# Optimization experiments

Measured on AMD Instinct MI355X. Metric: run time of the kernel, lower is better.

The kernel has to match this reference:

```python
import jax, jax.numpy as jnp
import numpy as np

B, T, S, I, H = 128, 256, 256, 512, 512


def setup_inputs() -> dict:
    key = jax.random.key(0)
    ks = jax.random.split(key, 10)
    sc = 0.02
    return {
        "x": jax.random.normal(ks[0], (B, T, I), jnp.float32),
        "h0": jax.random.normal(ks[1], (B, H), jnp.float32),
        "c0": jax.random.normal(ks[2], (B, H), jnp.float32),
        "ctx": jax.random.normal(ks[3], (S, B, H), jnp.float32),
        "Wi": jax.random.normal(ks[4], (4 * H, I), jnp.float32) * sc,
        "bi": jax.random.normal(ks[5], (4 * H,), jnp.float32) * sc,
        "Wh": jax.random.normal(ks[6], (4 * H, H), jnp.float32) * sc,
        "bh": jax.random.normal(ks[7], (4 * H,), jnp.float32) * sc,
        "W_in": jax.random.normal(ks[8], (H, H), jnp.float32) * sc,
        "W_out": jax.random.normal(ks[9], (H, 2 * H), jnp.float32) * sc,
    }


def reference(x, h0, c0, ctx, Wi, bi, Wh, bh, W_in, W_out):
    ctx_b = jnp.transpose(ctx, (1, 0, 2))  # [B, S, H]

    def step(carry, xt):
        hx, cx = carry
        gates = xt @ Wi.T + bi + hx @ Wh.T + bh  # [B, 4H]
        i_g, f_g, g_g, o_g = jnp.split(gates, 4, axis=1)
        cy = jax.nn.sigmoid(f_g) * cx + jax.nn.sigmoid(i_g) * jnp.tanh(g_g)
        hy = jax.nn.sigmoid(o_g) * jnp.tanh(cy)
        # soft dot attention
        target = hy @ W_in.T                              # [B, H]
        attn = jax.nn.softmax(jnp.einsum('bsh,bh->bs', ctx_b, target), axis=1)
        wc = jnp.einsum('bs,bsh->bh', attn, ctx_b)        # [B, H]
        h_tilde = jnp.tanh(jnp.concatenate([wc, hy], axis=1) @ W_out.T)
        return (h_tilde, cy), h_tilde

    (hf, cf), outs = jax.lax.scan(step, (h0, c0), jnp.transpose(x, (1, 0, 2)))
    output = jnp.transpose(outs, (1, 0, 2))  # [B, T, H] (batch_first)
    return output, hf, cf
```

## Files before the change

kernel.cpp:

```cpp
#include <hip/hip_runtime.h>
#include <hip/hip_bf16.h>
#include <stdint.h>

#define B_ 128
#define T_ 256
#define S_ 256
#define I_ 512
#define H_ 512
#define RSLOT 32

typedef __attribute__((ext_vector_type(8))) short short8;
typedef __attribute__((ext_vector_type(4))) float f32x4;
typedef unsigned short ushort_t;

__device__ __forceinline__ float bf2f(ushort_t u){
  union{ unsigned int i; float f;} v; v.i = ((unsigned int)u)<<16; return v.f;
}
__device__ __forceinline__ ushort_t f2bf(float f){
  union{ unsigned int i; float f;} v; v.f=f;
  unsigned int x=v.i; unsigned int r = x + 0x7fffu + ((x>>16)&1u);
  return (ushort_t)(r>>16);
}
__device__ __forceinline__ float sigm(float x){ return 1.f/(1.f + __expf(-x)); }
__device__ __forceinline__ float tanh_s(float x){
  float a = fabsf(x);
  float e = __expf(-2.f*a);
  float t = (1.f - e)/(1.f + e);
  return x < 0.f ? -t : t;
}

__device__ __forceinline__ f32x4 MFMA16(short8 a, short8 b, f32x4 c){
  typedef __attribute__((ext_vector_type(8))) __bf16 bf16x8;
  return __builtin_amdgcn_mfma_f32_16x16x32_bf16(
      __builtin_bit_cast(bf16x8, a), __builtin_bit_cast(bf16x8, b), c, 0, 0, 0);
}

__device__ __forceinline__ void fab_store_u64(ushort_t* p, unsigned long long v){
  __hip_atomic_store((unsigned long long*)p, v, __ATOMIC_RELAXED, __HIP_MEMORY_SCOPE_AGENT);
}


__global__ void k_cvt_bf16(const float* __restrict__ src, ushort_t* __restrict__ dst, int n){
  int i = (blockIdx.x*blockDim.x + threadIdx.x)*4;
  int stride = gridDim.x*blockDim.x*4;
  for (; i < n; i += stride){
    float4 v = *(const float4*)(src + i);
    ushort4 o; o.x=f2bf(v.x); o.y=f2bf(v.y); o.z=f2bf(v.z); o.w=f2bf(v.w);
    *(ushort4*)(dst + i) = o;
  }
}

__global__ void k_relayout_ctx2(const float* __restrict__ ctx, ushort_t* __restrict__ ctxh){
  int s = blockIdx.x >> 7;
  int b = blockIdx.x & 127;
  int tid = threadIdx.x;
  int h4 = tid*4;
  float4 v = *(const float4*)(ctx + ((size_t)s*128 + b)*512 + h4);
  ushort4 o; o.x=f2bf(v.x); o.y=f2bf(v.y); o.z=f2bf(v.z); o.w=f2bf(v.w);
  int half = tid >> 6, hh = h4 & 255;
  *(ushort4*)(ctxh + (((size_t)half*128 + b)*256 + s)*256 + hh) = o;
}

__global__ void k_transpose_512(const float* __restrict__ in, float* __restrict__ out){
  __shared__ float tile[32][33];
  int bx = blockIdx.x*32, by = blockIdx.y*32;
  int tx = threadIdx.x, ty = threadIdx.y;
  for (int r=0;r<32;r+=8) tile[ty+r][tx] = in[(by+ty+r)*512 + bx+tx];
  __syncthreads();
  for (int r=0;r<32;r+=8) out[(bx+ty+r)*512 + by+tx] = tile[tx][ty+r];
}

__global__ void k_init_state(const float* __restrict__ h0, const float* __restrict__ c0,
                             ushort_t* __restrict__ hring0, float* __restrict__ cyb){
  int i = blockIdx.x*blockDim.x + threadIdx.x;
  hring0[i] = f2bf(h0[i]);
  cyb[i] = c0[i];
}

__global__ void k_zero_bar(int* f){
  if (threadIdx.x < 256) f[threadIdx.x] = 0;
}

template<int BIAS, int SWAP>
__global__ __launch_bounds__(256) void k_gemm_bt(
    const float* __restrict__ A, const float* __restrict__ Bm,
    ushort_t* __restrict__ C, int M, int N, int K,
    const float* __restrict__ bias0, const float* __restrict__ bias1){
  __shared__ ushort_t Asm[128][40];
  __shared__ ushort_t Bsm[128][40];
  const int tid = threadIdx.x;
  const int mBase = blockIdx.x*128, nBase = blockIdx.y*128;
  const int l = tid & 63, wv = tid >> 6;
  const int wm = (wv>>1)*64, wn = (wv&1)*64;
  const int lr = l & 15, lq = l >> 4;
  const int srow = tid >> 1, scol = (tid & 1)*16;
  const float* Ap = A + (size_t)(mBase + srow)*K + scol;
  const float* Bp = Bm + (size_t)(nBase + srow)*K + scol;

  f32x4 acc[4][4];
  #pragma unroll
  for (int i=0;i<4;i++)
    #pragma unroll
    for (int j=0;j<4;j++) acc[i][j] = (f32x4)0.f;

  for (int k0 = 0; k0 < K; k0 += 32){
    float4 a0 = *(const float4*)(Ap + k0);
    float4 a1 = *(const float4*)(Ap + k0 + 4);
    float4 a2 = *(const float4*)(Ap + k0 + 8);
    float4 a3 = *(const float4*)(Ap + k0 + 12);
    float4 b0 = *(const float4*)(Bp + k0);
    float4 b1 = *(const float4*)(Bp + k0 + 4);
    float4 b2 = *(const float4*)(Bp + k0 + 8);
    float4 b3 = *(const float4*)(Bp + k0 + 12);
    __syncthreads();
    {
      ushort4 w;
      w.x=f2bf(a0.x); w.y=f2bf(a0.y); w.z=f2bf(a0.z); w.w=f2bf(a0.w);
      *(ushort4*)&Asm[srow][scol+0]  = w;
      w.x=f2bf(a1.x); w.y=f2bf(a1.y); w.z=f2bf(a1.z); w.w=f2bf(a1.w);
      *(ushort4*)&Asm[srow][scol+4]  = w;
      w.x=f2bf(a2.x); w.y=f2bf(a2.y); w.z=f2bf(a2.z); w.w=f2bf(a2.w);
      *(ushort4*)&Asm[srow][scol+8]  = w;
      w.x=f2bf(a3.x); w.y=f2bf(a3.y); w.z=f2bf(a3.z); w.w=f2bf(a3.w);
      *(ushort4*)&Asm[srow][scol+12] = w;
      w.x=f2bf(b0.x); w.y=f2bf(b0.y); w.z=f2bf(b0.z); w.w=f2bf(b0.w);
      *(ushort4*)&Bsm[srow][scol+0]  = w;
      w.x=f2bf(b1.x); w.y=f2bf(b1.y); w.z=f2bf(b1.z); w.w=f2bf(b1.w);
      *(ushort4*)&Bsm[srow][scol+4]  = w;
      w.x=f2bf(b2.x); w.y=f2bf(b2.y); w.z=f2bf(b2.z); w.w=f2bf(b2.w);
      *(ushort4*)&Bsm[srow][scol+8]  = w;
      w.x=f2bf(b3.x); w.y=f2bf(b3.y); w.z=f2bf(b3.z); w.w=f2bf(b3.w);
      *(ushort4*)&Bsm[srow][scol+12] = w;
    }
    __syncthreads();
    short8 aF[4], bF[4];
    #pragma unroll
    for (int i=0;i<4;i++) aF[i] = *(const short8*)&Asm[wm + i*16 + lr][lq*8];
    #pragma unroll
    for (int j=0;j<4;j++) bF[j] = *(const short8*)&Bsm[wn + j*16 + lr][lq*8];
    #pragma unroll
    for (int i=0;i<4;i++)
      #pragma unroll
      for (int j=0;j<4;j++)
        acc[i][j] = MFMA16(aF[i], bF[j], acc[i][j]);
  }

  #pragma unroll
  for (int j=0;j<4;j++){
    int col = nBase + wn + j*16 + lr;
    float bsum = 0.f;
    if (BIAS) bsum = bias0[col] + bias1[col];
    #pragma unroll
    for (int i=0;i<4;i++){
      int row0 = mBase + wm + i*16 + lq*4;
      #pragma unroll
      for (int r=0;r<4;r++){
        int row = row0 + r;
        size_t drow = SWAP ? ((size_t)(row & 127)*256 + (row >> 7)) : (size_t)row;
        C[drow*N + col] = f2bf(acc[i][j][r] + bsum);
      }
    }
  }
}

__device__ __forceinline__ void gbar(int* flags, int gen){
  __syncthreads();
  const int tid = threadIdx.x;
  if (tid == 0)
    __hip_atomic_store(&flags[blockIdx.x], gen, __ATOMIC_RELAXED, __HIP_MEMORY_SCOPE_AGENT);
  if (tid < 256){
    while (__hip_atomic_load(&flags[tid], __ATOMIC_RELAXED, __HIP_MEMORY_SCOPE_AGENT) < gen)
      __builtin_amdgcn_s_sleep(2);
  }
  __syncthreads();
  asm volatile("" ::: "memory");
}


__global__ __launch_bounds__(512, 1) void k_persist(
    const ushort_t* __restrict__ Xg, const ushort_t* __restrict__ C2b,
    const ushort_t* __restrict__ ctxh, const ushort_t* __restrict__ Whb,
    const ushort_t* __restrict__ Woutb,
    ushort_t* hring, ushort_t* hyring, ushort_t* wcring,
    float* cyb, float* out, float* hf, float* cf, int* flags)
{
  __shared__ union ShMem {
    struct { float red[8][256]; ushort_t pk[16][16]; } a;
    struct { float hy[512]; float sc[256]; float p[256]; float inv; float pad;
             float2 accs[512]; unsigned int pk32[128]; } b;
  } sh;

  const int pbid = blockIdx.x;
  const int tid = threadIdx.x;
  const int l = tid & 63, wv = tid >> 6;
  const int lr = l & 15, lq = l >> 4;
  int gen = 0;

  for (int t = 0; t < T_; ++t){
    const size_t slotC = (size_t)(t & (RSLOT-1)) * 65536;
    {
      const int bm = pbid >> 5, hc = pbid & 31;
      const int gate = wv & 3, khalf = wv >> 2;
      f32x4 acc = (f32x4)0.f;
      const ushort_t* ap = hring + slotC + (bm*16 + lr)*512 + khalf*256 + lq*8;
      const ushort_t* bp = Whb + (size_t)(gate*512 + hc*16 + lr)*512 + khalf*256 + lq*8;
      #pragma unroll
      for (int kk = 0; kk < 8; ++kk){
        short8 aF = *(const short8*)(ap + kk*32);
        short8 bF = *(const short8*)(bp + kk*32);
        acc = MFMA16(aF, bF, acc);
      }
      #pragma unroll
      for (int r = 0; r < 4; ++r) sh.a.red[wv][(lq*4 + r)*16 + lr] = acc[r];
      __syncthreads();
      if (tid < 256){
        const int b = bm*16 + (tid >> 4), h = hc*16 + (tid & 15);
        const ushort_t* xg = Xg + ((size_t)b*T_ + t)*2048 + h;
        float gi  = sh.a.red[0][tid] + sh.a.red[4][tid] + bf2f(xg[0]);
        float gf  = sh.a.red[1][tid] + sh.a.red[5][tid] + bf2f(xg[512]);
        float gg  = sh.a.red[2][tid] + sh.a.red[6][tid] + bf2f(xg[1024]);
        float go_ = sh.a.red[3][tid] + sh.a.red[7][tid] + bf2f(xg[1536]);
        float co = cyb[b*512 + h];
        float cn = sigm(gf)*co + sigm(gi)*tanh_s(gg);
        float hn = sigm(go_)*tanh_s(cn);
        cyb[b*512 + h] = cn;
        sh.a.pk[tid >> 4][tid & 15] = f2bf(hn);
        if (t == T_-1) cf[b*512 + h] = cn;
      }
      __syncthreads();
      if (tid < 64){
        int r = tid >> 2, c4 = tid & 3;
        unsigned long long v = *(unsigned long long*)&sh.a.pk[r][c4*4];
        fab_store_u64(hyring + slotC + (bm*16 + r)*512 + hc*16 + c4*4, v);
      }
    }
    gbar(flags, ++gen);

    {
      const int b = pbid >> 1, half = pbid & 1;
      if (tid < 128){
        ushort4 v = *(const ushort4*)(hyring + slotC + b*512 + tid*4);
        sh.b.hy[tid*4+0] = bf2f(v.x); sh.b.hy[tid*4+1] = bf2f(v.y);
        sh.b.hy[tid*4+2] = bf2f(v.z); sh.b.hy[tid*4+3] = bf2f(v.w);
      }
      __syncthreads();
      {
        float hv[8];
        #pragma unroll
        for (int e = 0; e < 8; ++e) hv[e] = sh.b.hy[l*8 + e];
        const ushort_t* c2p = C2b + (size_t)b*131072;
        #pragma unroll 2
        for (int i = 0; i < 32; ++i){
          int s = wv*32 + i;
          short8 cv = *(const short8*)(c2p + (size_t)s*512 + l*8);
          float d = 0.f;
          #pragma unroll
          for (int e = 0; e < 8; ++e) d += bf2f((ushort_t)cv[e]) * hv[e];
          #pragma unroll
          for (int off = 32; off; off >>= 1) d += __shfl_xor(d, off);
          if (l == 0) sh.b.sc[s] = d;
        }
      }
      __syncthreads();
      if (wv == 0){
        float v0 = sh.b.sc[l], v1 = sh.b.sc[l+64], v2 = sh.b.sc[l+128], v3 = sh.b.sc[l+192];
        float m = fmaxf(fmaxf(v0,v1), fmaxf(v2,v3));
        #pragma unroll
        for (int off = 32; off; off >>= 1) m = fmaxf(m, __shfl_xor(m, off));
        float e0=__expf(v0-m), e1=__expf(v1-m), e2=__expf(v2-m), e3=__expf(v3-m);
        float s4 = (e0+e1)+(e2+e3);
        #pragma unroll
        for (int off = 32; off; off >>= 1) s4 += __shfl_xor(s4, off);
        sh.b.p[l]=e0; sh.b.p[l+64]=e1; sh.b.p[l+128]=e2; sh.b.p[l+192]=e3;
        if (l == 0) sh.b.inv = 1.f/s4;
      }
      __syncthreads();
      {
        const int hp = tid & 127, sq = tid >> 7;
        const ushort_t* cxp = ctxh + (((size_t)half*128 + b)*256)*256;
        float2 a2 = make_float2(0.f, 0.f);
        #pragma unroll 4
        for (int j = 0; j < 64; ++j){
          int s = sq*64 + j;
          unsigned int uv = *(const unsigned int*)(cxp + (size_t)s*256 + hp*2);
          float pw = sh.b.p[s];
          a2.x += pw * bf2f((ushort_t)(uv & 0xffffu));
          a2.y += pw * bf2f((ushort_t)(uv >> 16));
        }
        sh.b.accs[tid] = a2;
      }
      __syncthreads();
      if (tid < 128){
        float inv = sh.b.inv;
        float2 a0 = sh.b.accs[tid],       a1 = sh.b.accs[tid + 128];
        float2 a2 = sh.b.accs[tid + 256], a3 = sh.b.accs[tid + 384];
        float x = (a0.x + a1.x + a2.x + a3.x)*inv;
        float y = (a0.y + a1.y + a2.y + a3.y)*inv;
        sh.b.pk32[tid] = (unsigned)f2bf(x) | ((unsigned)f2bf(y) << 16);
      }
      __syncthreads();
      if (tid < 64){
        unsigned long long v = *(unsigned long long*)&sh.b.pk32[tid*2];
        fab_store_u64(wcring + slotC + b*512 + half*256 + tid*4, v);
      }
    }
    gbar(flags, ++gen);

    {
      const int bm = pbid >> 5, nc = pbid & 31;
      f32x4 acc = (f32x4)0.f;
      const ushort_t* ap = (wv < 4 ? wcring : hyring) + slotC
                           + (bm*16 + lr)*512 + (wv & 3)*128 + lq*8;
      const ushort_t* bp = Woutb + (size_t)(nc*16 + lr)*1024 + wv*128 + lq*8;
      #pragma unroll
      for (int kk = 0; kk < 4; ++kk){
        short8 aF = *(const short8*)(ap + kk*32);
        short8 bF = *(const short8*)(bp + kk*32);
        acc = MFMA16(aF, bF, acc);
      }
      #pragma unroll
      for (int r = 0; r < 4; ++r) sh.a.red[wv][(lq*4 + r)*16 + lr] = acc[r];
      __syncthreads();
      if (tid < 256){
        float s = 0.f;
        #pragma unroll
        for (int w = 0; w < 8; ++w) s += sh.a.red[w][tid];
        float v = tanh_s(s);
        const int b = bm*16 + (tid >> 4), n = nc*16 + (tid & 15);
        out[((size_t)b*T_ + t)*512 + n] = v;
        sh.a.pk[tid >> 4][tid & 15] = f2bf(v);
        if (t == T_-1) hf[b*512 + n] = v;
      }
      __syncthreads();
      if (tid < 64){
        int r = tid >> 2, c4 = tid & 3;
        unsigned long long v = *(unsigned long long*)&sh.a.pk[r][c4*4];
        size_t slotN = (size_t)((t+1) & (RSLOT-1)) * 65536;
        fab_store_u64(hring + slotN + (bm*16 + r)*512 + nc*16 + c4*4, v);
      }
    }
    gbar(flags, ++gen);
  }
}


extern "C" void kernel_launch(void* const* d_in, const int* in_sizes, int n_in,
                              void* d_out, int out_size, void* d_ws, size_t ws_size,
                              hipStream_t stream){
  const float* x    = (const float*)d_in[0];
  const float* h0   = (const float*)d_in[1];
  const float* c0   = (const float*)d_in[2];
  const float* ctx  = (const float*)d_in[3];
  const float* Wi   = (const float*)d_in[4];
  const float* bi   = (const float*)d_in[5];
  const float* Wh   = (const float*)d_in[6];
  const float* bh   = (const float*)d_in[7];
  const float* Win  = (const float*)d_in[8];
  const float* Wout = (const float*)d_in[9];

  char* ws = (char*)d_ws;
  ushort_t* Xg     = (ushort_t*)(ws);
  ushort_t* C2b    = (ushort_t*)(ws + 134217728);
  ushort_t* ctxh   = (ushort_t*)(ws + 167772160);
  ushort_t* Whb    = (ushort_t*)(ws + 201326592);
  ushort_t* Woutb  = (ushort_t*)(ws + 203423744);
  float*    WinT   = (float*)   (ws + 204472320);
  ushort_t* hyring = (ushort_t*)(ws + 205520896);
  ushort_t* wcring = (ushort_t*)(ws + 209715200);
  ushort_t* hring  = (ushort_t*)(ws + 213909504);
  float*    cyb    = (float*)   (ws + 218103808);
  int*      flags  = (int*)     (ws + 218365952);

  float* out = (float*)d_out;
  float* hf  = out + (size_t)B_*T_*H_;
  float* cf  = hf + (size_t)B_*H_;

  k_relayout_ctx2<<<32768, 128, 0, stream>>>(ctx, ctxh);
  k_cvt_bf16<<<512, 256, 0, stream>>>(Wh, Whb, 4*H_*H_);
  k_cvt_bf16<<<512, 256, 0, stream>>>(Wout, Woutb, H_*2*H_);
  k_transpose_512<<<dim3(16,16), dim3(32,8), 0, stream>>>(Win, WinT);
  k_init_state<<<256, 256, 0, stream>>>(h0, c0, hring, cyb);
  k_zero_bar<<<1, 256, 0, stream>>>(flags);

  k_gemm_bt<1,0><<<dim3(256,16), 256, 0, stream>>>(x, Wi, Xg, B_*T_, 4*H_, I_, bi, bh);
  k_gemm_bt<0,1><<<dim3(256,4), 256, 0, stream>>>(ctx, WinT, C2b, S_*B_, H_, H_, nullptr, nullptr);

  k_persist<<<256, 512, 0, stream>>>(Xg, C2b, ctxh, Whb, Woutb,
                                     hring, hyring, wcring,
                                     cyb, out, hf, cf, flags);
}
```

Baseline: 10.67 ms.

## Keep recurrent weights in registers and batch context loads in persistent LSTM kernel

The Wh and Wout MFMA B-fragments are now loaded into registers once before the time loop instead of being re-read from global memory every step. The attention score loop issues its context loads in double-buffered batches of eight, and the weighted-context pass switches to a plain [B,S,H] bf16 layout with 16-byte loads and a 16-way shared-memory reduction. hy is read straight into registers without a shared staging pass. The cost is higher register pressure in a kernel whose grid-wide barrier needs all 256 blocks resident, and the launch bound drops its min-blocks hint.

```diff
diff --git a/kernel.cpp b/kernel.cpp
--- a/kernel.cpp
+++ b/kernel.cpp
@@ -50,15 +50,13 @@
   }
 }
 
-__global__ void k_relayout_ctx2(const float* __restrict__ ctx, ushort_t* __restrict__ ctxh){
+__global__ void k_relayout_ctx(const float* __restrict__ ctx, ushort_t* __restrict__ ctxb){
   int s = blockIdx.x >> 7;
   int b = blockIdx.x & 127;
-  int tid = threadIdx.x;
-  int h4 = tid*4;
+  int h4 = threadIdx.x * 4;
   float4 v = *(const float4*)(ctx + ((size_t)s*128 + b)*512 + h4);
   ushort4 o; o.x=f2bf(v.x); o.y=f2bf(v.y); o.z=f2bf(v.z); o.w=f2bf(v.w);
-  int half = tid >> 6, hh = h4 & 255;
-  *(ushort4*)(ctxh + (((size_t)half*128 + b)*256 + s)*256 + hh) = o;
+  *(ushort4*)(ctxb + ((size_t)b*256 + s)*512 + h4) = o;
 }
 
 __global__ void k_transpose_512(const float* __restrict__ in, float* __restrict__ out){
@@ -177,44 +175,56 @@
 }
 
 
-__global__ __launch_bounds__(512, 1) void k_persist(
+__global__ __launch_bounds__(512) void k_persist(
     const ushort_t* __restrict__ Xg, const ushort_t* __restrict__ C2b,
-    const ushort_t* __restrict__ ctxh, const ushort_t* __restrict__ Whb,
+    const ushort_t* __restrict__ ctxb, const ushort_t* __restrict__ Whb,
     const ushort_t* __restrict__ Woutb,
     ushort_t* hring, ushort_t* hyring, ushort_t* wcring,
     float* cyb, float* out, float* hf, float* cf, int* flags)
 {
-  __shared__ union ShMem {
-    struct { float red[8][256]; ushort_t pk[16][16]; } a;
-    struct { float hy[512]; float sc[256]; float p[256]; float inv; float pad;
-             float2 accs[512]; unsigned int pk32[128]; } b;
+  __shared__ union {
+    struct { float red[8][256]; ushort_t pk[256]; } a;
+    struct { float sc[256]; float p[256]; float inv;
+             float pacc[16][256]; ushort_t pk[256]; } b;
   } sh;
 
   const int pbid = blockIdx.x;
   const int tid = threadIdx.x;
   const int l = tid & 63, wv = tid >> 6;
   const int lr = l & 15, lq = l >> 4;
+
+  const int bm = pbid >> 5, hc = pbid & 31;
+  const int gate = wv & 3, khalf = wv >> 2;
+  short8 whr[8];
+  #pragma unroll
+  for (int kk=0;kk<8;kk++)
+    whr[kk] = *(const short8*)(Whb + (size_t)(gate*512 + hc*16 + lr)*512
+                               + khalf*256 + lq*8 + kk*32);
+  short8 wor[4];
+  #pragma unroll
+  for (int kk=0;kk<4;kk++)
+    wor[kk] = *(const short8*)(Woutb + (size_t)(hc*16 + lr)*1024
+                               + wv*128 + lq*8 + kk*32);
+
+  const int bB = pbid >> 1, half = pbid & 1;
+
   int gen = 0;
-
   for (int t = 0; t < T_; ++t){
     const size_t slotC = (size_t)(t & (RSLOT-1)) * 65536;
+
     {
-      const int bm = pbid >> 5, hc = pbid & 31;
-      const int gate = wv & 3, khalf = wv >> 2;
       f32x4 acc = (f32x4)0.f;
-      const ushort_t* ap = hring + slotC + (bm*16 + lr)*512 + khalf*256 + lq*8;
-      const ushort_t* bp = Whb + (size_t)(gate*512 + hc*16 + lr)*512 + khalf*256 + lq*8;
-      #pragma unroll
-      for (int kk = 0; kk < 8; ++kk){
-        short8 aF = *(const short8*)(ap + kk*32);
-        short8 bF = *(const short8*)(bp + kk*32);
-        acc = MFMA16(aF, bF, acc);
-      }
-      #pragma unroll
-      for (int r = 0; r < 4; ++r) sh.a.red[wv][(lq*4 + r)*16 + lr] = acc[r];
+      const ushort_t* ap = hring + slotC + (size_t)(bm*16 + lr)*512 + khalf*256 + lq*8;
+      short8 hv8[8];
+      #pragma unroll
+      for (int kk=0;kk<8;kk++) hv8[kk] = *(const short8*)(ap + kk*32);
+      #pragma unroll
+      for (int kk=0;kk<8;kk++) acc = MFMA16(hv8[kk], whr[kk], acc);
+      #pragma unroll
+      for (int r=0;r<4;r++) sh.a.red[wv][(lq*4+r)*16+lr] = acc[r];
       __syncthreads();
       if (tid < 256){
-        const int b = bm*16 + (tid >> 4), h = hc*16 + (tid & 15);
+        const int b = bm*16 + (tid>>4), h = hc*16 + (tid&15);
         const ushort_t* xg = Xg + ((size_t)b*T_ + t)*2048 + h;
         float gi  = sh.a.red[0][tid] + sh.a.red[4][tid] + bf2f(xg[0]);
         float gf  = sh.a.red[1][tid] + sh.a.red[5][tid] + bf2f(xg[512]);
@@ -224,119 +234,134 @@
         float cn = sigm(gf)*co + sigm(gi)*tanh_s(gg);
         float hn = sigm(go_)*tanh_s(cn);
         cyb[b*512 + h] = cn;
-        sh.a.pk[tid >> 4][tid & 15] = f2bf(hn);
+        sh.a.pk[tid] = f2bf(hn);
         if (t == T_-1) cf[b*512 + h] = cn;
       }
       __syncthreads();
       if (tid < 64){
-        int r = tid >> 2, c4 = tid & 3;
-        unsigned long long v = *(unsigned long long*)&sh.a.pk[r][c4*4];
-        fab_store_u64(hyring + slotC + (bm*16 + r)*512 + hc*16 + c4*4, v);
+        unsigned long long v = *(unsigned long long*)&sh.a.pk[tid*4];
+        fab_store_u64(hyring + slotC + (size_t)(bm*16 + (tid>>2))*512
+                      + hc*16 + (tid&3)*4, v);
       }
     }
     gbar(flags, ++gen);
 
     {
-      const int b = pbid >> 1, half = pbid & 1;
-      if (tid < 128){
-        ushort4 v = *(const ushort4*)(hyring + slotC + b*512 + tid*4);
-        sh.b.hy[tid*4+0] = bf2f(v.x); sh.b.hy[tid*4+1] = bf2f(v.y);
-        sh.b.hy[tid*4+2] = bf2f(v.z); sh.b.hy[tid*4+3] = bf2f(v.w);
-      }
-      __syncthreads();
+      float hv[8];
       {
-        float hv[8];
-        #pragma unroll
-        for (int e = 0; e < 8; ++e) hv[e] = sh.b.hy[l*8 + e];
-        const ushort_t* c2p = C2b + (size_t)b*131072;
-        #pragma unroll 2
-        for (int i = 0; i < 32; ++i){
-          int s = wv*32 + i;
-          short8 cv = *(const short8*)(c2p + (size_t)s*512 + l*8);
-          float d = 0.f;
+        short8 hvv = *(const short8*)(hyring + slotC + (size_t)bB*512 + l*8);
+        #pragma unroll
+        for (int e=0;e<8;e++) hv[e] = bf2f((ushort_t)hvv[e]);
+      }
+      {
+        const ushort_t* c2p = C2b + (size_t)bB*131072 + (size_t)(wv*32)*512 + l*8;
+        short8 ca[8], cb[8];
+        #pragma unroll
+        for (int j=0;j<8;j++) ca[j] = *(const short8*)(c2p + (size_t)j*512);
+        #pragma unroll
+        for (int c=0;c<4;c++){
+          if (c<3){
+            #pragma unroll
+            for (int j=0;j<8;j++){
+              short8 v = *(const short8*)(c2p + (size_t)((c+1)*8+j)*512);
+              if (c&1) ca[j]=v; else cb[j]=v;
+            }
+          }
           #pragma unroll
-          for (int e = 0; e < 8; ++e) d += bf2f((ushort_t)cv[e]) * hv[e];
-          #pragma unroll
-          for (int off = 32; off; off >>= 1) d += __shfl_xor(d, off);
-          if (l == 0) sh.b.sc[s] = d;
+          for (int j=0;j<8;j++){
+            short8 cv = (c&1)? cb[j] : ca[j];
+            float d = 0.f;
+            #pragma unroll
+            for (int e=0;e<8;e++) d += bf2f((ushort_t)cv[e]) * hv[e];
+            #pragma unroll
+            for (int off=32; off; off>>=1) d += __shfl_xor(d, off);
+            if (l==0) sh.b.sc[wv*32 + c*8 + j] = d;
+          }
         }
       }
       __syncthreads();
       if (wv == 0){
-        float v0 = sh.b.sc[l], v1 = sh.b.sc[l+64], v2 = sh.b.sc[l+128], v3 = sh.b.sc[l+192];
+        float v0=sh.b.sc[l], v1=sh.b.sc[l+64], v2=sh.b.sc[l+128], v3=sh.b.sc[l+192];
         float m = fmaxf(fmaxf(v0,v1), fmaxf(v2,v3));
         #pragma unroll
-        for (int off = 32; off; off >>= 1) m = fmaxf(m, __shfl_xor(m, off));
+        for (int off=32; off; off>>=1) m = fmaxf(m, __shfl_xor(m, off));
         float e0=__expf(v0-m), e1=__expf(v1-m), e2=__expf(v2-m), e3=__expf(v3-m);
         float s4 = (e0+e1)+(e2+e3);
         #pragma unroll
-        for (int off = 32; off; off >>= 1) s4 += __shfl_xor(s4, off);
+        for (int off=32; off; off>>=1) s4 += __shfl_xor(s4, off);
         sh.b.p[l]=e0; sh.b.p[l+64]=e1; sh.b.p[l+128]=e2; sh.b.p[l+192]=e3;
-        if (l == 0) sh.b.inv = 1.f/s4;
+        if (l==0) sh.b.inv = 1.f/s4;
       }
       __syncthreads();
       {
-        const int hp = tid & 127, sq = tid >> 7;
-        const ushort_t* cxp = ctxh + (((size_t)half*128 + b)*256)*256;
-        float2 a2 = make_float2(0.f, 0.f);
-        #pragma unroll 4
-        for (int j = 0; j < 64; ++j){
-          int s = sq*64 + j;
-          unsigned int uv = *(const unsigned int*)(cxp + (size_t)s*256 + hp*2);
-          float pw = sh.b.p[s];
-          a2.x += pw * bf2f((ushort_t)(uv & 0xffffu));
-          a2.y += pw * bf2f((ushort_t)(uv >> 16));
+        const int g = tid & 31, p = tid >> 5;
+        const ushort_t* cxp = ctxb + ((size_t)bB*256 + p*16)*512 + half*256 + g*8;
+        short8 va[8], vb[8];
+        #pragma unroll
+        for (int j=0;j<8;j++) va[j] = *(const short8*)(cxp + (size_t)j*512);
+        #pragma unroll
+        for (int j=0;j<8;j++) vb[j] = *(const short8*)(cxp + (size_t)(8+j)*512);
+        float a8[8];
+        #pragma unroll
+        for (int e=0;e<8;e++) a8[e]=0.f;
+        #pragma unroll
+        for (int j=0;j<8;j++){
+          float pw = sh.b.p[p*16 + j];
+          #pragma unroll
+          for (int e=0;e<8;e++) a8[e] += pw * bf2f((ushort_t)va[j][e]);
         }
-        sh.b.accs[tid] = a2;
-      }
-      __syncthreads();
-      if (tid < 128){
-        float inv = sh.b.inv;
-        float2 a0 = sh.b.accs[tid],       a1 = sh.b.accs[tid + 128];
-        float2 a2 = sh.b.accs[tid + 256], a3 = sh.b.accs[tid + 384];
-        float x = (a0.x + a1.x + a2.x + a3.x)*inv;
-        float y = (a0.y + a1.y + a2.y + a3.y)*inv;
-        sh.b.pk32[tid] = (unsigned)f2bf(x) | ((unsigned)f2bf(y) << 16);
+        #pragma unroll
+        for (int j=0;j<8;j++){
+          float pw = sh.b.p[p*16 + 8 + j];
+          #pragma unroll
+          for (int e=0;e<8;e++) a8[e] += pw * bf2f((ushort_t)vb[j][e]);
+        }
+        #pragma unroll
+        for (int e=0;e<8;e++) sh.b.pacc[p][g*8+e] = a8[e];
+      }
+      __syncthreads();
+      if (tid < 256){
+        float s = 0.f;
+        #pragma unroll
+        for (int p2=0;p2<16;p2++) s += sh.b.pacc[p2][tid];
+        sh.b.pk[tid] = f2bf(s * sh.b.inv);
       }
       __syncthreads();
       if (tid < 64){
-        unsigned long long v = *(unsigned long long*)&sh.b.pk32[tid*2];
-        fab_store_u64(wcring + slotC + b*512 + half*256 + tid*4, v);
+        unsigned long long v = *(unsigned long long*)&sh.b.pk[tid*4];
+        fab_store_u64(wcring + slotC + (size_t)bB*512 + half*256 + tid*4, v);
       }
     }
     gbar(flags, ++gen);
 
     {
-      const int bm = pbid >> 5, nc = pbid & 31;
       f32x4 acc = (f32x4)0.f;
       const ushort_t* ap = (wv < 4 ? wcring : hyring) + slotC
-                           + (bm*16 + lr)*512 + (wv & 3)*128 + lq*8;
-      const ushort_t* bp = Woutb + (size_t)(nc*16 + lr)*1024 + wv*128 + lq*8;
-      #pragma unroll
-      for (int kk = 0; kk < 4; ++kk){
-        short8 aF = *(const short8*)(ap + kk*32);
-        short8 bF = *(const short8*)(bp + kk*32);
-        acc = MFMA16(aF, bF, acc);
-      }
-      #pragma unroll
-      for (int r = 0; r < 4; ++r) sh.a.red[wv][(lq*4 + r)*16 + lr] = acc[r];
+                           + (size_t)(bm*16 + lr)*512 + (wv&3)*128 + lq*8;
+      short8 av[4];
+      #pragma unroll
+      for (int kk=0;kk<4;kk++) av[kk] = *(const short8*)(ap + kk*32);
+      #pragma unroll
+      for (int kk=0;kk<4;kk++) acc = MFMA16(av[kk], wor[kk], acc);
+      #pragma unroll
+      for (int r=0;r<4;r++) sh.a.red[wv][(lq*4+r)*16+lr] = acc[r];
       __syncthreads();
       if (tid < 256){
         float s = 0.f;
         #pragma unroll
-        for (int w = 0; w < 8; ++w) s += sh.a.red[w][tid];
+        for (int w=0;w<8;w++) s += sh.a.red[w][tid];
         float v = tanh_s(s);
-        const int b = bm*16 + (tid >> 4), n = nc*16 + (tid & 15);
+        const int b = bm*16 + (tid>>4), n = hc*16 + (tid&15);
         out[((size_t)b*T_ + t)*512 + n] = v;
-        sh.a.pk[tid >> 4][tid & 15] = f2bf(v);
+        sh.a.pk[tid] = f2bf(v);
         if (t == T_-1) hf[b*512 + n] = v;
       }
       __syncthreads();
       if (tid < 64){
-        int r = tid >> 2, c4 = tid & 3;
-        unsigned long long v = *(unsigned long long*)&sh.a.pk[r][c4*4];
+        unsigned long long v = *(unsigned long long*)&sh.a.pk[tid*4];
         size_t slotN = (size_t)((t+1) & (RSLOT-1)) * 65536;
-        fab_store_u64(hring + slotN + (bm*16 + r)*512 + nc*16 + c4*4, v);
+        fab_store_u64(hring + slotN + (size_t)(bm*16 + (tid>>2))*512
+                      + hc*16 + (tid&3)*4, v);
       }
     }
     gbar(flags, ++gen);
@@ -361,13 +386,13 @@
   char* ws = (char*)d_ws;
   ushort_t* Xg     = (ushort_t*)(ws);
   ushort_t* C2b    = (ushort_t*)(ws + 134217728);
-  ushort_t* ctxh   = (ushort_t*)(ws + 167772160);
+  ushort_t* ctxb   = (ushort_t*)(ws + 167772160);
   ushort_t* Whb    = (ushort_t*)(ws + 201326592);
   ushort_t* Woutb  = (ushort_t*)(ws + 203423744);
   float*    WinT   = (float*)   (ws + 204472320);
-  ushort_t* hyring = (ushort_t*)(ws + 205520896);
-  ushort_t* wcring = (ushort_t*)(ws + 209715200);
-  ushort_t* hring  = (ushort_t*)(ws + 213909504);
+  ushort_t* hring  = (ushort_t*)(ws + 205520896);
+  ushort_t* hyring = (ushort_t*)(ws + 209715200);
+  ushort_t* wcring = (ushort_t*)(ws + 213909504);
   float*    cyb    = (float*)   (ws + 218103808);
   int*      flags  = (int*)     (ws + 218365952);
 
@@ -375,7 +400,7 @@
   float* hf  = out + (size_t)B_*T_*H_;
   float* cf  = hf + (size_t)B_*H_;
 
-  k_relayout_ctx2<<<32768, 128, 0, stream>>>(ctx, ctxh);
+  k_relayout_ctx<<<32768, 128, 0, stream>>>(ctx, ctxb);
   k_cvt_bf16<<<512, 256, 0, stream>>>(Wh, Whb, 4*H_*H_);
   k_cvt_bf16<<<512, 256, 0, stream>>>(Wout, Woutb, H_*2*H_);
   k_transpose_512<<<dim3(16,16), dim3(32,8), 0, stream>>>(Win, WinT);
@@ -385,7 +410,7 @@
   k_gemm_bt<1,0><<<dim3(256,16), 256, 0, stream>>>(x, Wi, Xg, B_*T_, 4*H_, I_, bi, bh);
   k_gemm_bt<0,1><<<dim3(256,4), 256, 0, stream>>>(ctx, WinT, C2b, S_*B_, H_, H_, nullptr, nullptr);
 
-  k_persist<<<256, 512, 0, stream>>>(Xg, C2b, ctxh, Whb, Woutb,
+  k_persist<<<256, 512, 0, stream>>>(Xg, C2b, ctxb, Whb, Woutb,
                                      hring, hyring, wcring,
                                      cyb, out, hf, cf, flags);
 }
```

Result: faster. 9.044 ms (-15.2%).
